# Performance work log

Hardware: AMD Instinct MI355X
Metric: run time of the kernel (lower is better)

## Reference

```python
import jax, jax.numpy as jnp
import numpy as np

IN_DIM = 128
HID = 128
NUM_CLASSES = 10
N_NODES = 100000
N_EDGES = 1600000
NUM_GRAPHS = 128


def setup_inputs() -> dict:
    key = jax.random.key(0)
    ks = jax.random.split(key, 12)
    X = jax.random.normal(ks[0], (N_NODES, IN_DIM), dtype=jnp.float32)
    EI = jax.random.randint(ks[1], (2, N_EDGES), 0, N_NODES, dtype=jnp.int64)
    batch = jnp.sort(jax.random.randint(ks[2], (N_NODES,), 0, NUM_GRAPHS, dtype=jnp.int64))
    s_in = 1.0 / np.sqrt(IN_DIM)
    s_h = 1.0 / np.sqrt(HID)
    s_m = 1.0 / np.sqrt(2 * HID)
    params = {
        'W1': jax.random.uniform(ks[3], (IN_DIM, HID), jnp.float32, -s_in, s_in),
        'b1': jnp.zeros((HID,), jnp.float32),
        'W2': jax.random.uniform(ks[4], (HID, HID), jnp.float32, -s_h, s_h),
        'b2': jnp.zeros((HID,), jnp.float32),
        'W3': jax.random.uniform(ks[5], (HID, HID), jnp.float32, -s_h, s_h),
        'b3': jnp.zeros((HID,), jnp.float32),
        'Wm1': jax.random.uniform(ks[6], (2 * HID, HID), jnp.float32, -s_m, s_m),
        'bm1': jnp.zeros((HID,), jnp.float32),
        'Wm2': jax.random.uniform(ks[7], (HID, NUM_CLASSES), jnp.float32, -s_h, s_h),
        'bm2': jnp.zeros((NUM_CLASSES,), jnp.float32),
    }
    return dict(X=X, EI=EI, batch=batch, num_graphs=NUM_GRAPHS, **params)


def _gcn_norm(EI, n):
    # add self loops, compute D^{-1/2}[row] * D^{-1/2}[col]
    loops = jnp.arange(n, dtype=EI.dtype)
    row = jnp.concatenate([EI[0], loops])
    col = jnp.concatenate([EI[1], loops])
    deg = jax.ops.segment_sum(jnp.ones_like(row, dtype=jnp.float32), row, num_segments=n)
    dis = (deg + 1e-12) ** -0.5
    norm = dis[row] * dis[col]
    return row, col, norm


def _gcn_layer(x, row, col, norm, W, b):
    h = x @ W + b                       # [N, out]
    msg = h[col] * norm[:, None]        # gather + scale  [E+N, out]
    return jax.ops.segment_sum(msg, row, num_segments=x.shape[0])  # scatter-add


def _pool_mean_max(x, batch, num_graphs):
    s = jax.ops.segment_sum(x, batch, num_segments=num_graphs)
    cnt = jax.ops.segment_sum(jnp.ones((x.shape[0],), x.dtype), batch, num_segments=num_graphs)
    mean = s / (cnt[:, None] + 1e-12)
    mx = jax.ops.segment_max(x, batch, num_segments=num_graphs)
    return jnp.concatenate([mean, mx], axis=1)


def reference(X, EI, batch, num_graphs, W1, b1, W2, b2, W3, b3, Wm1, bm1, Wm2, bm2):
    n = X.shape[0]
    row, col, norm = _gcn_norm(EI, n)
    x = jax.nn.relu(_gcn_layer(X, row, col, norm, W1, b1))
    x = jax.nn.relu(_gcn_layer(x, row, col, norm, W2, b2))
    x = jax.nn.relu(_gcn_layer(x, row, col, norm, W3, b3))
    g = _pool_mean_max(x, batch, num_graphs)
    h = jax.nn.relu(g @ Wm1 + bm1)
    return h @ Wm2 + bm2
```

## Files before the change

### kernel.cpp

```cpp
#include <hip/hip_runtime.h>
#include <hip/hip_fp16.h>
#include <cstdint>
#include <cstddef>

#define DIM 128
#define NG 128
#define NCLS 10
#define PSLICE 8
#define CPAD 64
#define NOWN 256
#define RPB 391
#define NPBLK 1024
#define WTBLK 192
#define OCAP 16
#define OVCAP 65536

typedef _Float16 f16;
typedef __attribute__((ext_vector_type(8))) _Float16 f16x8;
typedef __attribute__((ext_vector_type(4))) float f32x4;
typedef __attribute__((ext_vector_type(4))) unsigned u32x4;


__global__ __launch_bounds__(256) void k_part(
    const int* __restrict__ rw, const int* __restrict__ cl, int E,
    unsigned* __restrict__ buckets, int* __restrict__ bcnt,
    unsigned long long* __restrict__ ovf, int* __restrict__ ovfn,
    const float* __restrict__ W1, const float* __restrict__ W2,
    const float* __restrict__ W3, __half* __restrict__ Wt1,
    __half* __restrict__ Wt2, __half* __restrict__ Wt3) {
  if (blockIdx.x >= NPBLK) {
    int gi = (blockIdx.x - NPBLK) * 256 + threadIdx.x;
    int m = gi / (DIM * DIM);
    int i = gi % (DIM * DIM);
    const float* W = (m == 0) ? W1 : (m == 1) ? W2 : W3;
    __half* Wt = (m == 0) ? Wt1 : (m == 1) ? Wt2 : Wt3;
    int k = i >> 7, c = i & 127;
    Wt[(size_t)c * DIM + k] = __float2half(W[(size_t)k * DIM + c]);
    return;
  }
  __shared__ int lcnt[NOWN];
  if (threadIdx.x < NOWN) lcnt[threadIdx.x] = 0;
  __syncthreads();
  int b = blockIdx.x;
  int C = (((E + NPBLK - 1) / NPBLK + 3) & ~3);
  int s = b * C;
  int e = s + C;
  if (e > E) e = E;
  auto put = [&](int r, int c) {
    int o = (unsigned)r / RPB;
    int li = r - o * RPB;
    int sl = atomicAdd(&lcnt[o], 1);
    if (sl < OCAP) {
      buckets[((size_t)o * NPBLK + b) * OCAP + sl] =
          ((unsigned)li << 17) | (unsigned)c;
    } else {
      int oi = atomicAdd(ovfn, 1);
      if (oi < OVCAP)
        ovf[oi] = ((unsigned long long)(unsigned)r << 32) | (unsigned)c;
    }
  };
  for (int i = s + (int)threadIdx.x * 4; i < e; i += 1024) {
    if (i + 3 < e) {
      int4 r4 = *(const int4*)(rw + i);
      int4 c4 = *(const int4*)(cl + i);
      put(r4.x, c4.x);
      put(r4.y, c4.y);
      put(r4.z, c4.z);
      put(r4.w, c4.w);
    } else {
      for (int j = i; j < e; ++j) put(rw[j], cl[j]);
    }
  }
  __syncthreads();
  if (threadIdx.x < NOWN) {
    int v = lcnt[threadIdx.x];
    bcnt[threadIdx.x * NPBLK + b] = v < OCAP ? v : OCAP;
  }
}

__global__ __launch_bounds__(256) void k_place(
    const unsigned* __restrict__ buckets, const int* __restrict__ bcnt,
    const unsigned long long* __restrict__ ovf, const int* __restrict__ ovfn,
    int* __restrict__ cnt, float* __restrict__ dis, int* __restrict__ csrc,
    int N) {
  extern __shared__ int sm[];
  int* lcnt = sm;
  int* csr = sm + ((RPB + 3) & ~3);
  int o = blockIdx.x;
  int r0 = o * RPB;
  int rows = N - r0;
  if (rows > RPB) rows = RPB;
  if (rows <= 0) return;
  for (int i = threadIdx.x; i < rows; i += 256) lcnt[i] = 0;
  __syncthreads();
  const int* bc = bcnt + o * NPBLK;
  const unsigned* bp = buckets + (size_t)o * NPBLK * OCAP;
  for (int j = (int)threadIdx.x; j < NPBLK * OCAP; j += 256) {
    int seg = j >> 4;
    int pos = j & 15;
    if (pos < bc[seg]) {
      unsigned ent = bp[j];
      int li = (int)(ent >> 17);
      int c = (int)(ent & 0x1ffffu);
      int sl = atomicAdd(&lcnt[li], 1);
      if (sl < CPAD) csr[(li << 6) + sl] = c;
    }
  }
  int nov = *ovfn;
  if (nov > OVCAP) nov = OVCAP;
  for (int j = (int)threadIdx.x; j < nov; j += 256) {
    unsigned long long ent = ovf[j];
    int r = (int)(unsigned)(ent >> 32);
    int li = r - r0;
    if (li >= 0 && li < rows) {
      int c = (int)(unsigned)(ent & 0xffffffffu);
      int sl = atomicAdd(&lcnt[li], 1);
      if (sl < CPAD) csr[(li << 6) + sl] = c;
    }
  }
  __syncthreads();
  u32x4* dst = (u32x4*)(csrc + ((size_t)r0 << 6));
  const u32x4* src = (const u32x4*)csr;
  int n4 = rows * 16;
  for (int j = (int)threadIdx.x; j < n4; j += 256)
    __builtin_nontemporal_store(src[j], dst + j);
  for (int i = threadIdx.x; i < rows; i += 256) {
    int v = lcnt[i];
    cnt[r0 + i] = v;
    dis[r0 + i] = rsqrtf((float)(v + 1));
  }
}


template <int FP32IN>
__global__ __launch_bounds__(256, 3) void k_gemm(
    const void* __restrict__ Ain, const __half* __restrict__ Wt,
    const float* __restrict__ bias, const float* __restrict__ dis,
    __half* __restrict__ Hh, int N) {
  int t = threadIdx.x;
  int lane = t & 63;
  int wv = t >> 6;
  int l15 = lane & 15, lg = lane >> 4;
  int cb = (wv & 1) * 64;

  f16x8 bfr[4][4];
#pragma unroll
  for (int ct = 0; ct < 4; ++ct) {
    int c = cb + ct * 16 + l15;
    const f16* wp = (const f16*)Wt + (size_t)c * DIM + lg * 8;
#pragma unroll
    for (int ks = 0; ks < 4; ++ks) bfr[ks][ct] = *(const f16x8*)(wp + ks * 32);
  }
  float bv[4];
#pragma unroll
  for (int ct = 0; ct < 4; ++ct) bv[ct] = bias[cb + ct * 16 + l15];

  const int nt2 = (N + 31) / 32;
  for (int t2 = blockIdx.x; t2 < nt2; t2 += gridDim.x) {
    int row0 = t2 * 32 + (wv >> 1) * 16;
    int rA = row0 + l15;
    if (rA > N - 1) rA = N - 1;
    f16x8 afr[4];
    if constexpr (FP32IN) {
      const float* ap = (const float*)Ain + (size_t)rA * DIM + lg * 8;
#pragma unroll
      for (int ks = 0; ks < 4; ++ks) {
        float4 v0 = *(const float4*)(ap + ks * 32);
        float4 v1 = *(const float4*)(ap + ks * 32 + 4);
        f16x8 a;
        a[0] = (f16)v0.x; a[1] = (f16)v0.y; a[2] = (f16)v0.z; a[3] = (f16)v0.w;
        a[4] = (f16)v1.x; a[5] = (f16)v1.y; a[6] = (f16)v1.z; a[7] = (f16)v1.w;
        afr[ks] = a;
      }
    } else {
      const f16* ap = (const f16*)Ain + (size_t)rA * DIM + lg * 8;
#pragma unroll
      for (int ks = 0; ks < 4; ++ks) afr[ks] = *(const f16x8*)(ap + ks * 32);
    }

    f32x4 acc[4];
#pragma unroll
    for (int ct = 0; ct < 4; ++ct) acc[ct] = (f32x4){0.f, 0.f, 0.f, 0.f};
#pragma unroll
    for (int ks = 0; ks < 4; ++ks)
#pragma unroll
      for (int ct = 0; ct < 4; ++ct)
        acc[ct] = __builtin_amdgcn_mfma_f32_16x16x32_f16(afr[ks], bfr[ks][ct], acc[ct], 0, 0, 0);

#pragma unroll
    for (int j = 0; j < 4; ++j) {
      int r = row0 + lg * 4 + j;
      if (r < N) {
        float dr = dis[r];
#pragma unroll
        for (int ct = 0; ct < 4; ++ct) {
          float o = (acc[ct][j] + bv[ct]) * dr;
          Hh[(size_t)r * DIM + cb + ct * 16 + l15] = __float2half(o);
        }
      }
    }
  }
}


template <int STORE_NT>
__global__ __launch_bounds__(256) void k_agg(
    const __half* __restrict__ Hh, __half* __restrict__ Ah,
    const int* __restrict__ csrc, const int* __restrict__ cntA,
    const float* __restrict__ dis, int N) {
  int wave = (int)(((size_t)blockIdx.x * blockDim.x + threadIdx.x) >> 6);
  int lane = threadIdx.x & 63;
  int g = lane >> 4;
  int q = lane & 15;
  int r = wave * 4 + g;
  if (r >= N) return;
  int cnt = cntA[r];
  if (cnt > CPAD) cnt = CPAD;
  float dr = dis[r];
  const int* cp = csrc + ((size_t)r << 6);
  const f16* hb = (const f16*)Hh + q * 8;

  float4 aA0 = {0,0,0,0}, aA1 = {0,0,0,0};
  float4 aB0 = {0,0,0,0}, aB1 = {0,0,0,0};
  float4 aC0 = {0,0,0,0}, aC1 = {0,0,0,0};
  float4 aD0 = {0,0,0,0}, aD1 = {0,0,0,0};

#define ACC8(u, x0, x1)                                                   \
  {                                                                       \
    float2 f_;                                                            \
    f_ = __half22float2(*reinterpret_cast<const __half2*>(&(u).x));       \
    x0.x += f_.x; x0.y += f_.y;                                           \
    f_ = __half22float2(*reinterpret_cast<const __half2*>(&(u).y));       \
    x0.z += f_.x; x0.w += f_.y;                                           \
    f_ = __half22float2(*reinterpret_cast<const __half2*>(&(u).z));       \
    x1.x += f_.x; x1.y += f_.y;                                           \
    f_ = __half22float2(*reinterpret_cast<const __half2*>(&(u).w));       \
    x1.z += f_.x; x1.w += f_.y;                                           \
  }

  int i = 0;
  for (; i + 3 < cnt; i += 4) {
    int c0 = cp[i], c1 = cp[i + 1], c2 = cp[i + 2], c3 = cp[i + 3];
    uint4 u0 = *(const uint4*)(hb + (size_t)c0 * DIM);
    uint4 u1 = *(const uint4*)(hb + (size_t)c1 * DIM);
    uint4 u2 = *(const uint4*)(hb + (size_t)c2 * DIM);
    uint4 u3 = *(const uint4*)(hb + (size_t)c3 * DIM);
    ACC8(u0, aA0, aA1);
    ACC8(u1, aB0, aB1);
    ACC8(u2, aC0, aC1);
    ACC8(u3, aD0, aD1);
  }
  for (; i < cnt; ++i) {
    int c0 = cp[i];
    uint4 u0 = *(const uint4*)(hb + (size_t)c0 * DIM);
    ACC8(u0, aA0, aA1);
  }
  {
    uint4 us = *(const uint4*)(hb + (size_t)r * DIM);
    ACC8(us, aA0, aA1);
  }
#undef ACC8
  float4 s0, s1;
  s0.x = (aA0.x + aB0.x) + (aC0.x + aD0.x);
  s0.y = (aA0.y + aB0.y) + (aC0.y + aD0.y);
  s0.z = (aA0.z + aB0.z) + (aC0.z + aD0.z);
  s0.w = (aA0.w + aB0.w) + (aC0.w + aD0.w);
  s1.x = (aA1.x + aB1.x) + (aC1.x + aD1.x);
  s1.y = (aA1.y + aB1.y) + (aC1.y + aD1.y);
  s1.z = (aA1.z + aB1.z) + (aC1.z + aD1.z);
  s1.w = (aA1.w + aB1.w) + (aC1.w + aD1.w);
  float o0 = fmaxf(dr * s0.x, 0.f), o1 = fmaxf(dr * s0.y, 0.f);
  float o2 = fmaxf(dr * s0.z, 0.f), o3 = fmaxf(dr * s0.w, 0.f);
  float o4 = fmaxf(dr * s1.x, 0.f), o5 = fmaxf(dr * s1.y, 0.f);
  float o6 = fmaxf(dr * s1.z, 0.f), o7 = fmaxf(dr * s1.w, 0.f);
  __half2 p0 = __floats2half2_rn(o0, o1);
  __half2 p1 = __floats2half2_rn(o2, o3);
  __half2 p2 = __floats2half2_rn(o4, o5);
  __half2 p3 = __floats2half2_rn(o6, o7);
  u32x4 u;
  u.x = *(unsigned int*)&p0;
  u.y = *(unsigned int*)&p1;
  u.z = *(unsigned int*)&p2;
  u.w = *(unsigned int*)&p3;
  u32x4* dst = (u32x4*)((f16*)Ah + (size_t)r * DIM + q * 8);
  if constexpr (STORE_NT) {
    __builtin_nontemporal_store(u, dst);
  } else {
    *dst = u;
  }
}


__device__ __forceinline__ int lower_bound_batch(const int* batch, int N, int g) {
  int lo = 0, hi = N;
  while (lo < hi) {
    int mid = (lo + hi) >> 1;
    if (batch[mid] < g) lo = mid + 1; else hi = mid;
  }
  return lo;
}

__global__ void k_pool1(const __half* __restrict__ A, const int* __restrict__ batch,
                        int N, float* __restrict__ part) {
  int g = blockIdx.x / PSLICE, sl = blockIdx.x % PSLICE;
  int c = threadIdx.x;
  int s = lower_bound_batch(batch, N, g);
  int e = lower_bound_batch(batch, N, g + 1);
  int len = e - s;
  int ns = s + (len * sl) / PSLICE;
  int ne = s + (len * (sl + 1)) / PSLICE;
  float sum = 0.f, mx = -INFINITY;
  for (int n = ns; n < ne; ++n) {
    float v = __half2float(A[(size_t)n * DIM + c]);
    sum += v;
    mx = fmaxf(mx, v);
  }
  part[((size_t)(g * PSLICE + sl) * 2 + 0) * DIM + c] = sum;
  part[((size_t)(g * PSLICE + sl) * 2 + 1) * DIM + c] = mx;
}

__global__ void k_head(const float* __restrict__ part, const int* __restrict__ batch,
                       int N, const float* __restrict__ Wm1,
                       const float* __restrict__ bm1, const float* __restrict__ Wm2,
                       const float* __restrict__ bm2, float* __restrict__ out) {
  __shared__ float gs[256];
  __shared__ float hs[DIM];
  int g = blockIdx.x;
  int c = threadIdx.x;
  float sum = 0.f, mx = -INFINITY;
  for (int sl = 0; sl < PSLICE; ++sl) {
    sum += part[((size_t)(g * PSLICE + sl) * 2 + 0) * DIM + c];
    mx = fmaxf(mx, part[((size_t)(g * PSLICE + sl) * 2 + 1) * DIM + c]);
  }
  int s = lower_bound_batch(batch, N, g);
  int e = lower_bound_batch(batch, N, g + 1);
  gs[c] = sum / ((float)(e - s) + 1e-12f);
  gs[c + 128] = mx;
  __syncthreads();
  float acc = bm1[c];
#pragma unroll 8
  for (int k = 0; k < 256; ++k) acc = fmaf(gs[k], Wm1[k * DIM + c], acc);
  hs[c] = fmaxf(acc, 0.f);
  __syncthreads();
  if (c < NCLS) {
    float a2 = bm2[c];
#pragma unroll 8
    for (int k = 0; k < DIM; ++k) a2 = fmaf(hs[k], Wm2[k * NCLS + c], a2);
    out[(size_t)g * NCLS + c] = a2;
  }
}


static inline size_t al256(size_t x) { return (x + 255) & ~(size_t)255; }

extern "C" void kernel_launch(void* const* d_in, const int* in_sizes, int n_in,
                              void* d_out, int out_size, void* d_ws, size_t ws_size,
                              hipStream_t stream) {
  const float* X = (const float*)d_in[0];
  const int* EI = (const int*)d_in[1];
  const int* batch = (const int*)d_in[2];
  const float* W1 = (const float*)d_in[4];
  const float* b1 = (const float*)d_in[5];
  const float* W2 = (const float*)d_in[6];
  const float* b2 = (const float*)d_in[7];
  const float* W3 = (const float*)d_in[8];
  const float* b3 = (const float*)d_in[9];
  const float* Wm1 = (const float*)d_in[10];
  const float* bm1 = (const float*)d_in[11];
  const float* Wm2 = (const float*)d_in[12];
  const float* bm2 = (const float*)d_in[13];
  float* OUT = (float*)d_out;

  const int N = in_sizes[0] / DIM;
  const int E = in_sizes[1] / 2;
  const int G = NG;

  const int* EI_row = EI;
  const int* EI_col = EI + E;

  char* p = (char*)d_ws;
  size_t off = 0;
  auto take = [&](size_t bytes) { void* r = p + off; off = al256(off + bytes); return r; };

  int* cnt = (int*)take((size_t)N * 4);
  int* bcnt = (int*)take((size_t)NOWN * NPBLK * 4);
  int* ovfn = (int*)take(256);
  unsigned long long* ovf = (unsigned long long*)take((size_t)OVCAP * 8);
  float* dis = (float*)take((size_t)N * 4);
  int* csrc = (int*)take((size_t)N * CPAD * 4);
  unsigned* buckets = (unsigned*)take((size_t)NOWN * NPBLK * OCAP * 4);
  __half* Hh = (__half*)take((size_t)N * DIM * 2);
  __half* Ah = (__half*)take((size_t)N * DIM * 2);
  __half* Wt1 = (__half*)take((size_t)DIM * DIM * 2);
  __half* Wt2 = (__half*)take((size_t)DIM * DIM * 2);
  __half* Wt3 = (__half*)take((size_t)DIM * DIM * 2);
  float* part = (float*)take((size_t)G * PSLICE * 2 * DIM * 4);
  (void)ws_size; (void)n_in; (void)out_size;

  hipMemsetAsync(ovfn, 0, 4, stream);

  k_part<<<NPBLK + WTBLK, 256, 0, stream>>>(EI_row, EI_col, E, buckets, bcnt,
                                            ovf, ovfn, W1, W2, W3, Wt1, Wt2, Wt3);
  const int placeLds = ((RPB + 3) & ~3) * 4 + RPB * 64 * 4;
  k_place<<<NOWN, 256, placeLds, stream>>>(buckets, bcnt, ovf, ovfn, cnt, dis, csrc, N);

  const int aggBlocks = (N * 16 + 255) / 256;

  k_gemm<1><<<512, 256, 0, stream>>>(X, Wt1, b1, dis, Hh, N);
  k_agg<0><<<aggBlocks, 256, 0, stream>>>(Hh, Ah, csrc, cnt, dis, N);
  k_gemm<0><<<512, 256, 0, stream>>>(Ah, Wt2, b2, dis, Hh, N);
  k_agg<0><<<aggBlocks, 256, 0, stream>>>(Hh, Ah, csrc, cnt, dis, N);
  k_gemm<0><<<512, 256, 0, stream>>>(Ah, Wt3, b3, dis, Hh, N);
  k_agg<1><<<aggBlocks, 256, 0, stream>>>(Hh, Ah, csrc, cnt, dis, N);

  k_pool1<<<G * PSLICE, DIM, 0, stream>>>(Ah, batch, N, part);
  k_head<<<G, DIM, 0, stream>>>(part, batch, N, Wm1, bm1, Wm2, bm2, OUT);
}
```

Before: 378.3 us.

## Fuse aggregation with next layer GEMM via LDS tile, drop nontemporal stores

Adds a k_agge kernel where each 256-thread block aggregates 16 rows into shared memory, then immediately runs the next layer's 128x128 MFMA GEMM on that tile. Layers 2 and 3 no longer write and re-read the intermediate aggregated activations through global memory, and the standalone k_gemm launches for those layers go away. Ping-pong HA/HB buffers are introduced. Nontemporal stores are also replaced with regular stores in k_place and k_agg. Risk: each block reloads the full weight matrix and runs a small 16-row MFMA tile, which may lower GEMM efficiency.

```diff
diff --git a/kernel.cpp b/kernel.cpp
--- a/kernel.cpp
+++ b/kernel.cpp
@@ -122,8 +122,7 @@
   u32x4* dst = (u32x4*)(csrc + ((size_t)r0 << 6));
   const u32x4* src = (const u32x4*)csr;
   int n4 = rows * 16;
-  for (int j = (int)threadIdx.x; j < n4; j += 256)
-    __builtin_nontemporal_store(src[j], dst + j);
+  for (int j = (int)threadIdx.x; j < n4; j += 256) dst[j] = src[j];
   for (int i = threadIdx.x; i < rows; i += 256) {
     int v = lcnt[i];
     cnt[r0 + i] = v;
@@ -202,8 +201,130 @@
   }
 }
 
-
-template <int STORE_NT>
+#define ACC8(u, x0, x1)                                                   \
+  {                                                                       \
+    float2 f_;                                                            \
+    f_ = __half22float2(*reinterpret_cast<const __half2*>(&(u).x));       \
+    x0.x += f_.x; x0.y += f_.y;                                           \
+    f_ = __half22float2(*reinterpret_cast<const __half2*>(&(u).y));       \
+    x0.z += f_.x; x0.w += f_.y;                                           \
+    f_ = __half22float2(*reinterpret_cast<const __half2*>(&(u).z));       \
+    x1.x += f_.x; x1.y += f_.y;                                           \
+    f_ = __half22float2(*reinterpret_cast<const __half2*>(&(u).w));       \
+    x1.z += f_.x; x1.w += f_.y;                                           \
+  }
+
+
+__global__ __launch_bounds__(256, 4) void k_agge(
+    const __half* __restrict__ Hh, const __half* __restrict__ Wt,
+    const float* __restrict__ bias, const float* __restrict__ dis,
+    __half* __restrict__ Ho, const int* __restrict__ csrc,
+    const int* __restrict__ cntA, int N) {
+  __shared__ f16 smA[16][136];
+  int t = threadIdx.x;
+  int lane = t & 63;
+  int wv = t >> 6;
+  {
+    int g = lane >> 4;
+    int q = lane & 15;
+    int rowin = wv * 4 + g;
+    int r = blockIdx.x * 16 + rowin;
+    if (r < N) {
+      int cnt = cntA[r];
+      if (cnt > CPAD) cnt = CPAD;
+      float dr = dis[r];
+      const int* cp = csrc + ((size_t)r << 6);
+      const f16* hb = (const f16*)Hh + q * 8;
+      float4 aA0 = {0,0,0,0}, aA1 = {0,0,0,0};
+      float4 aB0 = {0,0,0,0}, aB1 = {0,0,0,0};
+      float4 aC0 = {0,0,0,0}, aC1 = {0,0,0,0};
+      float4 aD0 = {0,0,0,0}, aD1 = {0,0,0,0};
+      int i = 0;
+      for (; i + 3 < cnt; i += 4) {
+        int c0 = cp[i], c1 = cp[i + 1], c2 = cp[i + 2], c3 = cp[i + 3];
+        uint4 u0 = *(const uint4*)(hb + (size_t)c0 * DIM);
+        uint4 u1 = *(const uint4*)(hb + (size_t)c1 * DIM);
+        uint4 u2 = *(const uint4*)(hb + (size_t)c2 * DIM);
+        uint4 u3 = *(const uint4*)(hb + (size_t)c3 * DIM);
+        ACC8(u0, aA0, aA1);
+        ACC8(u1, aB0, aB1);
+        ACC8(u2, aC0, aC1);
+        ACC8(u3, aD0, aD1);
+      }
+      for (; i < cnt; ++i) {
+        int c0 = cp[i];
+        uint4 u0 = *(const uint4*)(hb + (size_t)c0 * DIM);
+        ACC8(u0, aA0, aA1);
+      }
+      {
+        uint4 us = *(const uint4*)(hb + (size_t)r * DIM);
+        ACC8(us, aA0, aA1);
+      }
+      float s0x = (aA0.x + aB0.x) + (aC0.x + aD0.x);
+      float s0y = (aA0.y + aB0.y) + (aC0.y + aD0.y);
+      float s0z = (aA0.z + aB0.z) + (aC0.z + aD0.z);
+      float s0w = (aA0.w + aB0.w) + (aC0.w + aD0.w);
+      float s1x = (aA1.x + aB1.x) + (aC1.x + aD1.x);
+      float s1y = (aA1.y + aB1.y) + (aC1.y + aD1.y);
+      float s1z = (aA1.z + aB1.z) + (aC1.z + aD1.z);
+      float s1w = (aA1.w + aB1.w) + (aC1.w + aD1.w);
+      __half2 p0 = __floats2half2_rn(fmaxf(dr * s0x, 0.f), fmaxf(dr * s0y, 0.f));
+      __half2 p1 = __floats2half2_rn(fmaxf(dr * s0z, 0.f), fmaxf(dr * s0w, 0.f));
+      __half2 p2 = __floats2half2_rn(fmaxf(dr * s1x, 0.f), fmaxf(dr * s1y, 0.f));
+      __half2 p3 = __floats2half2_rn(fmaxf(dr * s1z, 0.f), fmaxf(dr * s1w, 0.f));
+      uint4 u;
+      u.x = *(unsigned int*)&p0;
+      u.y = *(unsigned int*)&p1;
+      u.z = *(unsigned int*)&p2;
+      u.w = *(unsigned int*)&p3;
+      *(uint4*)&smA[rowin][q * 8] = u;
+    } else {
+      *(uint4*)&smA[rowin][q * 8] = make_uint4(0, 0, 0, 0);
+    }
+  }
+  __syncthreads();
+  {
+    int l15 = lane & 15, lg = lane >> 4;
+    int cb = wv * 32;
+    f16x8 bfr[4][2];
+#pragma unroll
+    for (int ct = 0; ct < 2; ++ct) {
+      int c = cb + ct * 16 + l15;
+      const f16* wp = (const f16*)Wt + (size_t)c * DIM + lg * 8;
+#pragma unroll
+      for (int ks = 0; ks < 4; ++ks) bfr[ks][ct] = *(const f16x8*)(wp + ks * 32);
+    }
+    float bv[2];
+#pragma unroll
+    for (int ct = 0; ct < 2; ++ct) bv[ct] = bias[cb + ct * 16 + l15];
+    f16x8 afr[4];
+#pragma unroll
+    for (int ks = 0; ks < 4; ++ks)
+      afr[ks] = *(const f16x8*)&smA[l15][ks * 32 + lg * 8];
+    f32x4 acc[2];
+#pragma unroll
+    for (int ct = 0; ct < 2; ++ct) acc[ct] = (f32x4){0.f, 0.f, 0.f, 0.f};
+#pragma unroll
+    for (int ks = 0; ks < 4; ++ks)
+#pragma unroll
+      for (int ct = 0; ct < 2; ++ct)
+        acc[ct] = __builtin_amdgcn_mfma_f32_16x16x32_f16(afr[ks], bfr[ks][ct], acc[ct], 0, 0, 0);
+#pragma unroll
+    for (int j = 0; j < 4; ++j) {
+      int r = blockIdx.x * 16 + lg * 4 + j;
+      if (r < N) {
+        float dr = dis[r];
+#pragma unroll
+        for (int ct = 0; ct < 2; ++ct) {
+          float o = (acc[ct][j] + bv[ct]) * dr;
+          Ho[(size_t)r * DIM + cb + ct * 16 + l15] = __float2half(o);
+        }
+      }
+    }
+  }
+}
+
+
 __global__ __launch_bounds__(256) void k_agg(
     const __half* __restrict__ Hh, __half* __restrict__ Ah,
     const int* __restrict__ csrc, const int* __restrict__ cntA,
@@ -219,25 +340,10 @@
   float dr = dis[r];
   const int* cp = csrc + ((size_t)r << 6);
   const f16* hb = (const f16*)Hh + q * 8;
-
   float4 aA0 = {0,0,0,0}, aA1 = {0,0,0,0};
   float4 aB0 = {0,0,0,0}, aB1 = {0,0,0,0};
   float4 aC0 = {0,0,0,0}, aC1 = {0,0,0,0};
   float4 aD0 = {0,0,0,0}, aD1 = {0,0,0,0};
-
-#define ACC8(u, x0, x1)                                                   \
-  {                                                                       \
-    float2 f_;                                                            \
-    f_ = __half22float2(*reinterpret_cast<const __half2*>(&(u).x));       \
-    x0.x += f_.x; x0.y += f_.y;                                           \
-    f_ = __half22float2(*reinterpret_cast<const __half2*>(&(u).y));       \
-    x0.z += f_.x; x0.w += f_.y;                                           \
-    f_ = __half22float2(*reinterpret_cast<const __half2*>(&(u).z));       \
-    x1.x += f_.x; x1.y += f_.y;                                           \
-    f_ = __half22float2(*reinterpret_cast<const __half2*>(&(u).w));       \
-    x1.z += f_.x; x1.w += f_.y;                                           \
-  }
-
   int i = 0;
   for (; i + 3 < cnt; i += 4) {
     int c0 = cp[i], c1 = cp[i + 1], c2 = cp[i + 2], c3 = cp[i + 3];
@@ -259,36 +365,26 @@
     uint4 us = *(const uint4*)(hb + (size_t)r * DIM);
     ACC8(us, aA0, aA1);
   }
-#undef ACC8
-  float4 s0, s1;
-  s0.x = (aA0.x + aB0.x) + (aC0.x + aD0.x);
-  s0.y = (aA0.y + aB0.y) + (aC0.y + aD0.y);
-  s0.z = (aA0.z + aB0.z) + (aC0.z + aD0.z);
-  s0.w = (aA0.w + aB0.w) + (aC0.w + aD0.w);
-  s1.x = (aA1.x + aB1.x) + (aC1.x + aD1.x);
-  s1.y = (aA1.y + aB1.y) + (aC1.y + aD1.y);
-  s1.z = (aA1.z + aB1.z) + (aC1.z + aD1.z);
-  s1.w = (aA1.w + aB1.w) + (aC1.w + aD1.w);
-  float o0 = fmaxf(dr * s0.x, 0.f), o1 = fmaxf(dr * s0.y, 0.f);
-  float o2 = fmaxf(dr * s0.z, 0.f), o3 = fmaxf(dr * s0.w, 0.f);
-  float o4 = fmaxf(dr * s1.x, 0.f), o5 = fmaxf(dr * s1.y, 0.f);
-  float o6 = fmaxf(dr * s1.z, 0.f), o7 = fmaxf(dr * s1.w, 0.f);
-  __half2 p0 = __floats2half2_rn(o0, o1);
-  __half2 p1 = __floats2half2_rn(o2, o3);
-  __half2 p2 = __floats2half2_rn(o4, o5);
-  __half2 p3 = __floats2half2_rn(o6, o7);
-  u32x4 u;
+  float s0x = (aA0.x + aB0.x) + (aC0.x + aD0.x);
+  float s0y = (aA0.y + aB0.y) + (aC0.y + aD0.y);
+  float s0z = (aA0.z + aB0.z) + (aC0.z + aD0.z);
+  float s0w = (aA0.w + aB0.w) + (aC0.w + aD0.w);
+  float s1x = (aA1.x + aB1.x) + (aC1.x + aD1.x);
+  float s1y = (aA1.y + aB1.y) + (aC1.y + aD1.y);
+  float s1z = (aA1.z + aB1.z) + (aC1.z + aD1.z);
+  float s1w = (aA1.w + aB1.w) + (aC1.w + aD1.w);
+  __half2 p0 = __floats2half2_rn(fmaxf(dr * s0x, 0.f), fmaxf(dr * s0y, 0.f));
+  __half2 p1 = __floats2half2_rn(fmaxf(dr * s0z, 0.f), fmaxf(dr * s0w, 0.f));
+  __half2 p2 = __floats2half2_rn(fmaxf(dr * s1x, 0.f), fmaxf(dr * s1y, 0.f));
+  __half2 p3 = __floats2half2_rn(fmaxf(dr * s1z, 0.f), fmaxf(dr * s1w, 0.f));
+  uint4 u;
   u.x = *(unsigned int*)&p0;
   u.y = *(unsigned int*)&p1;
   u.z = *(unsigned int*)&p2;
   u.w = *(unsigned int*)&p3;
-  u32x4* dst = (u32x4*)((f16*)Ah + (size_t)r * DIM + q * 8);
-  if constexpr (STORE_NT) {
-    __builtin_nontemporal_store(u, dst);
-  } else {
-    *dst = u;
-  }
-}
+  *(uint4*)((f16*)Ah + (size_t)r * DIM + q * 8) = u;
+}
+#undef ACC8
 
 
 __device__ __forceinline__ int lower_bound_batch(const int* batch, int N, int g) {
@@ -389,7 +485,8 @@
   float* dis = (float*)take((size_t)N * 4);
   int* csrc = (int*)take((size_t)N * CPAD * 4);
   unsigned* buckets = (unsigned*)take((size_t)NOWN * NPBLK * OCAP * 4);
-  __half* Hh = (__half*)take((size_t)N * DIM * 2);
+  __half* HA = (__half*)take((size_t)N * DIM * 2);
+  __half* HB = (__half*)take((size_t)N * DIM * 2);
   __half* Ah = (__half*)take((size_t)N * DIM * 2);
   __half* Wt1 = (__half*)take((size_t)DIM * DIM * 2);
   __half* Wt2 = (__half*)take((size_t)DIM * DIM * 2);
@@ -404,14 +501,13 @@
   const int placeLds = ((RPB + 3) & ~3) * 4 + RPB * 64 * 4;
   k_place<<<NOWN, 256, placeLds, stream>>>(buckets, bcnt, ovf, ovfn, cnt, dis, csrc, N);
 
+  const int tiles16 = (N + 15) / 16;
   const int aggBlocks = (N * 16 + 255) / 256;
 
-  k_gemm<1><<<512, 256, 0, stream>>>(X, Wt1, b1, dis, Hh, N);
-  k_agg<0><<<aggBlocks, 256, 0, stream>>>(Hh, Ah, csrc, cnt, dis, N);
-  k_gemm<0><<<512, 256, 0, stream>>>(Ah, Wt2, b2, dis, Hh, N);
-  k_agg<0><<<aggBlocks, 256, 0, stream>>>(Hh, Ah, csrc, cnt, dis, N);
-  k_gemm<0><<<512, 256, 0, stream>>>(Ah, Wt3, b3, dis, Hh, N);
-  k_agg<1><<<aggBlocks, 256, 0, stream>>>(Hh, Ah, csrc, cnt, dis, N);
+  k_gemm<1><<<512, 256, 0, stream>>>(X, Wt1, b1, dis, HA, N);
+  k_agge<<<tiles16, 256, 0, stream>>>(HA, Wt2, b2, dis, HB, csrc, cnt, N);
+  k_agge<<<tiles16, 256, 0, stream>>>(HB, Wt3, b3, dis, HA, csrc, cnt, N);
+  k_agg<<<aggBlocks, 256, 0, stream>>>(HA, Ah, csrc, cnt, dis, N);
 
   k_pool1<<<G * PSLICE, DIM, 0, stream>>>(Ah, batch, N, part);
   k_head<<<G, DIM, 0, stream>>>(part, batch, N, Wm1, bm1, Wm2, bm2, OUT);
```

Result: faster. 368.3 us (-2.6%).
